# Kernel tuning notes

Hardware: AMD Instinct MI355X
Metric: run time of the kernel (lower is better)

The kernel has to match this reference:

```python
import jax, jax.numpy as jnp
import numpy as np

B, T, C = 1024, 256, 512
HEAD = 64

def setup_inputs() -> dict:
    key = jax.random.key(0)
    kx, kq, kk, kv = jax.random.split(key, 4)
    x = jax.random.normal(kx, (B, T, C), dtype=jnp.float32)
    # nn.Linear(n_embed, head_size, bias=False): y = x @ W where W is [C, head]
    s = 1.0 / np.sqrt(C)
    Wq = jax.random.normal(kq, (C, HEAD), dtype=jnp.float32) * s
    Wk = jax.random.normal(kk, (C, HEAD), dtype=jnp.float32) * s
    Wv = jax.random.normal(kv, (C, HEAD), dtype=jnp.float32) * s
    return {"x": x, "Wq": Wq, "Wk": Wk, "Wv": Wv}

def reference(x, Wq, Wk, Wv):
    # Naive single-head causal self-attention (dropout in eval mode = identity).
    T_ = x.shape[1]
    q = jnp.einsum('btc,ch->bth', x, Wq)
    k = jnp.einsum('btc,ch->bth', x, Wk)
    v = jnp.einsum('btc,ch->bth', x, Wv)
    scale = q.shape[-1] ** -0.5
    wei = jnp.einsum('bth,bsh->bts', q, k) * scale  # [B,T,T]
    causal = jnp.tril(jnp.ones((T_, T_), dtype=bool))
    wei = jnp.where(causal, wei, -jnp.inf)
    wei = jax.nn.softmax(wei, axis=-1)
    out = jnp.einsum('bts,bsh->bth', wei, v)  # [B,T,HEAD]
    return out
```

## Files before the change

### kernel.cpp

```cpp
#include <hip/hip_runtime.h>
#include <hip/hip_bf16.h>

#define NB 1024
#define NT 256
#define NC 512
#define NH 64

typedef __attribute__((ext_vector_type(8))) short bf16x8;
typedef __attribute__((ext_vector_type(4))) float f32x4;
typedef __attribute__((ext_vector_type(4))) short s16x4;
typedef __attribute__((ext_vector_type(4))) int   i32x4;

__device__ __forceinline__ short f2bf(float f) {
    unsigned u = __builtin_bit_cast(unsigned, f);
    u = (u + 0x7FFFu + ((u >> 16) & 1u)) >> 16;
    return (short)u;
}

__device__ __forceinline__ bf16x8 cvt8(f32x4 a0, f32x4 a1) {
#if defined(__has_builtin) && __has_builtin(__builtin_amdgcn_cvt_pk_bf16_f32)
    i32x4 pk;
    pk[0] = __builtin_bit_cast(int, __builtin_amdgcn_cvt_pk_bf16_f32(a0[0], a0[1]));
    pk[1] = __builtin_bit_cast(int, __builtin_amdgcn_cvt_pk_bf16_f32(a0[2], a0[3]));
    pk[2] = __builtin_bit_cast(int, __builtin_amdgcn_cvt_pk_bf16_f32(a1[0], a1[1]));
    pk[3] = __builtin_bit_cast(int, __builtin_amdgcn_cvt_pk_bf16_f32(a1[2], a1[3]));
    return __builtin_bit_cast(bf16x8, pk);
#else
    bf16x8 r;
    r[0] = f2bf(a0[0]); r[1] = f2bf(a0[1]); r[2] = f2bf(a0[2]); r[3] = f2bf(a0[3]);
    r[4] = f2bf(a1[0]); r[5] = f2bf(a1[1]); r[6] = f2bf(a1[2]); r[7] = f2bf(a1[3]);
    return r;
#endif
}

__global__ void swzw(const float* __restrict__ Wq, const float* __restrict__ Wk,
                     const float* __restrict__ Wv, short* __restrict__ wsw) {
    int tid = blockIdx.x * 256 + threadIdx.x;
    int j    = tid & 7;
    int l16  = (tid >> 3) & 15;
    int quad = (tid >> 7) & 3;
    int tgi  = (tid >> 9) & 3;
    int c    = (tid >> 11) & 15;
    int g2   = tid >> 15;
    const float* W = (g2 == 0) ? Wq : (g2 == 1) ? Wk : Wv;
    int h = tgi * 16 + l16;
    int k = c * 32 + quad * 8 + j;
    wsw[tid] = f2bf(W[k * NH + h]);
}

__global__ __launch_bounds__(512, 4)
void attn_fused(const float* __restrict__ x, const short* __restrict__ wsw,
                float* __restrict__ out) {
    __shared__ short lds[36864];
    const int b    = blockIdx.x;
    const int tid  = threadIdx.x;
    const int w    = tid >> 6;
    const int lane = tid & 63;
    const int l16  = lane & 15;
    const int quad = lane >> 4;

    const float* xb = x + (size_t)b * NT * NC;
    const int rts[2] = { w, 15 - w };

    short* pbw = lds + w * 512;
    const short* kb = lds + 4096;
    const short* vb = lds + 20480;

    bf16x8 qf[2][2];

    #pragma unroll
    for (int i = 0; i < 2; ++i) {
        const int R = rts[i];
        const float* xp = xb + (size_t)(R * 16 + l16) * NC + quad * 8;
        const short* wq = wsw + lane * 8;

        f32x4 acc[12];
        #pragma unroll
        for (int t = 0; t < 12; ++t) acc[t] = (f32x4){0.f, 0.f, 0.f, 0.f};

        f32x4 xa[2][2];
        xa[0][0] = *(const f32x4*)xp;
        xa[0][1] = *(const f32x4*)(xp + 4);

        #pragma unroll 2
        for (int c = 0; c < 16; ++c) {
            const int cur = c & 1;
            if (c < 15) {
                const float* pn = xp + (c + 1) * 32;
                xa[cur ^ 1][0] = *(const f32x4*)pn;
                xa[cur ^ 1][1] = *(const f32x4*)(pn + 4);
            }
            const short* wc = wq + c * 2048;
            bf16x8 af = cvt8(xa[cur][0], xa[cur][1]);
            {
                bf16x8 b0 = *(const bf16x8*)(wc);
                bf16x8 b1 = *(const bf16x8*)(wc + 512);
                bf16x8 b2 = *(const bf16x8*)(wc + 1024);
                bf16x8 b3 = *(const bf16x8*)(wc + 1536);
                acc[0] = __builtin_amdgcn_mfma_f32_16x16x32_bf16(af, b0, acc[0], 0, 0, 0);
                acc[1] = __builtin_amdgcn_mfma_f32_16x16x32_bf16(af, b1, acc[1], 0, 0, 0);
                acc[2] = __builtin_amdgcn_mfma_f32_16x16x32_bf16(af, b2, acc[2], 0, 0, 0);
                acc[3] = __builtin_amdgcn_mfma_f32_16x16x32_bf16(af, b3, acc[3], 0, 0, 0);
            }
            {
                bf16x8 b4 = *(const bf16x8*)(wc + 32768);
                bf16x8 b5 = *(const bf16x8*)(wc + 33280);
                bf16x8 b6 = *(const bf16x8*)(wc + 33792);
                bf16x8 b7 = *(const bf16x8*)(wc + 34304);
                acc[4] = __builtin_amdgcn_mfma_f32_16x16x32_bf16(af, b4, acc[4], 0, 0, 0);
                acc[5] = __builtin_amdgcn_mfma_f32_16x16x32_bf16(af, b5, acc[5], 0, 0, 0);
                acc[6] = __builtin_amdgcn_mfma_f32_16x16x32_bf16(af, b6, acc[6], 0, 0, 0);
                acc[7] = __builtin_amdgcn_mfma_f32_16x16x32_bf16(af, b7, acc[7], 0, 0, 0);
            }
            {
                bf16x8 b8  = *(const bf16x8*)(wc + 65536);
                bf16x8 b9  = *(const bf16x8*)(wc + 66048);
                bf16x8 b10 = *(const bf16x8*)(wc + 66560);
                bf16x8 b11 = *(const bf16x8*)(wc + 67072);
                acc[8]  = __builtin_amdgcn_mfma_f32_16x16x32_bf16(af, b8,  acc[8],  0, 0, 0);
                acc[9]  = __builtin_amdgcn_mfma_f32_16x16x32_bf16(af, b9,  acc[9],  0, 0, 0);
                acc[10] = __builtin_amdgcn_mfma_f32_16x16x32_bf16(af, b10, acc[10], 0, 0, 0);
                acc[11] = __builtin_amdgcn_mfma_f32_16x16x32_bf16(af, b11, acc[11], 0, 0, 0);
            }
        }

        #pragma unroll
        for (int hh = 0; hh < 2; ++hh) {
            #pragma unroll
            for (int t2 = 0; t2 < 2; ++t2) {
                const f32x4 a = acc[hh * 2 + t2];
                #pragma unroll
                for (int r = 0; r < 4; ++r)
                    pbw[(quad * 4 + r) * 32 + t2 * 16 + l16] = f2bf(a[r] * 0.125f);
            }
            qf[i][hh] = *(const bf16x8*)(pbw + l16 * 32 + quad * 8);
        }
        #pragma unroll
        for (int t2 = 0; t2 < 4; ++t2) {
            const int h = t2 * 16 + l16;
            const int koff = 4096 + R * 1024 + (h >> 5) * 512 + ((h >> 3) & 3) * 128 + (h & 7);
            const f32x4 a = acc[4 + t2];
            #pragma unroll
            for (int r = 0; r < 4; ++r)
                lds[koff + (quad * 4 + r) * 8] = f2bf(a[r]);
        }
        #pragma unroll
        for (int t2 = 0; t2 < 4; ++t2) {
            const int h = t2 * 16 + l16;
            const f32x4 a = acc[8 + t2];
            #pragma unroll
            for (int r = 0; r < 4; ++r) {
                const int row = R * 16 + quad * 4 + r;
                lds[20480 + (row >> 5) * 2048 + (h >> 4) * 512 + ((row >> 3) & 3) * 128
                    + (h & 15) * 8 + (row & 7)] = f2bf(a[r]);
            }
        }
    }
    __syncthreads();

    #pragma unroll
    for (int i = 0; i < 2; ++i) {
        const int R = rts[i];
        f32x4 sacc[16];
        #pragma unroll
        for (int ct = 0; ct < 16; ++ct) sacc[ct] = (f32x4){0.f, 0.f, 0.f, 0.f};

        #pragma unroll
        for (int ct = 0; ct < 16; ++ct) {
            if (ct <= R) {
                #pragma unroll
                for (int c = 0; c < 2; ++c) {
                    bf16x8 kf = *(const bf16x8*)(kb + ct * 1024 + c * 512 + quad * 128 + l16 * 8);
                    sacc[ct] = __builtin_amdgcn_mfma_f32_16x16x32_bf16(kf, qf[i][c], sacc[ct], 0, 0, 0);
                }
                if (ct == R) {
                    #pragma unroll
                    for (int r = 0; r < 4; ++r)
                        if (quad * 4 + r > l16) sacc[ct][r] = -1e30f;
                }
            }
        }

        f32x4 mm = (f32x4){-1e30f, -1e30f, -1e30f, -1e30f};
        #pragma unroll
        for (int ct = 0; ct < 16; ++ct)
            if (ct <= R) {
                #pragma unroll
                for (int r = 0; r < 4; ++r) mm[r] = fmaxf(mm[r], sacc[ct][r]);
            }
        float m0 = fmaxf(fmaxf(mm[0], mm[1]), fmaxf(mm[2], mm[3]));
        m0 = fmaxf(m0, __shfl_xor(m0, 16));
        m0 = fmaxf(m0, __shfl_xor(m0, 32));

        f32x4 lsv = (f32x4){0.f, 0.f, 0.f, 0.f};
        #pragma unroll
        for (int ct = 0; ct < 16; ++ct)
            if (ct <= R) {
                #pragma unroll
                for (int r = 0; r < 4; ++r) {
                    float p = __expf(sacc[ct][r] - m0);
                    sacc[ct][r] = p;
                    lsv[r] += p;
                }
            }
        float ls = (lsv[0] + lsv[1]) + (lsv[2] + lsv[3]);
        ls += __shfl_xor(ls, 16);
        ls += __shfl_xor(ls, 32);

        f32x4 oacc[4];
        #pragma unroll
        for (int ot = 0; ot < 4; ++ot) oacc[ot] = (f32x4){0.f, 0.f, 0.f, 0.f};

        #pragma unroll
        for (int c2 = 0; c2 < 8; ++c2) {
            if (c2 <= (R >> 1)) {
                #pragma unroll
                for (int half = 0; half < 2; ++half) {
                    int ct = 2 * c2 + half;
                    s16x4 vals;
                    if (ct <= R) {
                        #pragma unroll
                        for (int r = 0; r < 4; ++r) vals[r] = f2bf(sacc[ct][r]);
                    } else {
                        vals = (s16x4){0, 0, 0, 0};
                    }
                    *(s16x4*)(pbw + l16 * 32 + half * 16 + quad * 4) = vals;
                }
                bf16x8 pf = *(const bf16x8*)(pbw + l16 * 32 + quad * 8);
                #pragma unroll
                for (int ot = 0; ot < 4; ++ot) {
                    bf16x8 vf = *(const bf16x8*)(vb + c2 * 2048 + ot * 512 + quad * 128 + l16 * 8);
                    oacc[ot] = __builtin_amdgcn_mfma_f32_16x16x32_bf16(vf, pf, oacc[ot], 0, 0, 0);
                }
            }
        }

        float inv = 1.0f / ls;
        float* ob = out + ((size_t)b * NT + R * 16 + l16) * NH;
        #pragma unroll
        for (int ot = 0; ot < 4; ++ot) {
            f32x4 o;
            #pragma unroll
            for (int r = 0; r < 4; ++r) o[r] = oacc[ot][r] * inv;
            *(f32x4*)(ob + ot * 16 + quad * 4) = o;
        }
    }
}

extern "C" void kernel_launch(void* const* d_in, const int* in_sizes, int n_in,
                              void* d_out, int out_size, void* d_ws, size_t ws_size,
                              hipStream_t stream) {
    const float* x  = (const float*)d_in[0];
    const float* Wq = (const float*)d_in[1];
    const float* Wk = (const float*)d_in[2];
    const float* Wv = (const float*)d_in[3];
    float* outp = (float*)d_out;
    short* wsw  = (short*)d_ws;

    swzw<<<384, 256, 0, stream>>>(Wq, Wk, Wv, wsw);
    attn_fused<<<NB, 512, 0, stream>>>(x, wsw, outp);
}
```

Measured before the change: 776.5 us.

## Reuse weight fragments across both row tiles by splitting QKV projection into two passes

The projection phase is restructured so each wave processes both of its row tiles at once, loading each weight fragment once and feeding it to two MFMAs. The 12 output column tiles are split into two passes of six, and the weight buffer is re-swizzled into a pass-major layout so each pass reads contiguous fragments. This halves weight loads per wave and keeps the accumulator count at twelve, but x rows are now read twice (once per pass). The per-wave scratch stride is also padded from 32 to 40 shorts to cut LDS bank conflicts, which enlarges the shared buffer slightly.

```diff
diff --git a/kernel.cpp b/kernel.cpp
--- a/kernel.cpp
+++ b/kernel.cpp
@@ -39,10 +39,18 @@
     int j    = tid & 7;
     int l16  = (tid >> 3) & 15;
     int quad = (tid >> 7) & 3;
-    int tgi  = (tid >> 9) & 3;
-    int c    = (tid >> 11) & 15;
-    int g2   = tid >> 15;
-    const float* W = (g2 == 0) ? Wq : (g2 == 1) ? Wk : Wv;
+    int rest = tid >> 9;
+    int tl   = rest % 6;
+    int cp   = rest / 6;
+    int c    = cp & 15;
+    int pass = cp >> 4;
+    int g, tgi;
+    if (pass == 0) {
+        if (tl < 4) { g = 0; tgi = tl; } else { g = 1; tgi = tl - 4; }
+    } else {
+        if (tl < 2) { g = 1; tgi = tl + 2; } else { g = 2; tgi = tl - 2; }
+    }
+    const float* W = (g == 0) ? Wq : (g == 1) ? Wk : Wv;
     int h = tgi * 16 + l16;
     int k = c * 32 + quad * 8 + j;
     wsw[tid] = f2bf(W[k * NH + h]);
@@ -51,7 +59,7 @@
 __global__ __launch_bounds__(512, 4)
 void attn_fused(const float* __restrict__ x, const short* __restrict__ wsw,
                 float* __restrict__ out) {
-    __shared__ short lds[36864];
+    __shared__ short lds[37888];
     const int b    = blockIdx.x;
     const int tid  = threadIdx.x;
     const int w    = tid >> 6;
@@ -62,97 +70,124 @@
     const float* xb = x + (size_t)b * NT * NC;
     const int rts[2] = { w, 15 - w };
 
-    short* pbw = lds + w * 512;
-    const short* kb = lds + 4096;
-    const short* vb = lds + 20480;
+    short* pbw = lds + w * 640;
+    const short* kb = lds + 5120;
+    const short* vb = lds + 21504;
 
     bf16x8 qf[2][2];
 
+    const float* xp0 = xb + (size_t)(rts[0] * 16 + l16) * NC + quad * 8;
+    const float* xp1 = xb + (size_t)(rts[1] * 16 + l16) * NC + quad * 8;
+
     #pragma unroll
-    for (int i = 0; i < 2; ++i) {
-        const int R = rts[i];
-        const float* xp = xb + (size_t)(R * 16 + l16) * NC + quad * 8;
-        const short* wq = wsw + lane * 8;
-
-        f32x4 acc[12];
-        #pragma unroll
-        for (int t = 0; t < 12; ++t) acc[t] = (f32x4){0.f, 0.f, 0.f, 0.f};
-
-        f32x4 xa[2][2];
-        xa[0][0] = *(const f32x4*)xp;
-        xa[0][1] = *(const f32x4*)(xp + 4);
+    for (int pass = 0; pass < 2; ++pass) {
+        f32x4 acc[2][6];
+        #pragma unroll
+        for (int rt = 0; rt < 2; ++rt)
+            #pragma unroll
+            for (int t = 0; t < 6; ++t)
+                acc[rt][t] = (f32x4){0.f, 0.f, 0.f, 0.f};
+
+        const short* wp = wsw + pass * 49152 + lane * 8;
+
+        f32x4 xa[2][2][2];
+        xa[0][0][0] = *(const f32x4*)xp0;
+        xa[0][0][1] = *(const f32x4*)(xp0 + 4);
+        xa[0][1][0] = *(const f32x4*)xp1;
+        xa[0][1][1] = *(const f32x4*)(xp1 + 4);
 
         #pragma unroll 2
         for (int c = 0; c < 16; ++c) {
             const int cur = c & 1;
             if (c < 15) {
-                const float* pn = xp + (c + 1) * 32;
-                xa[cur ^ 1][0] = *(const f32x4*)pn;
-                xa[cur ^ 1][1] = *(const f32x4*)(pn + 4);
-            }
-            const short* wc = wq + c * 2048;
-            bf16x8 af = cvt8(xa[cur][0], xa[cur][1]);
+                const float* p0 = xp0 + (c + 1) * 32;
+                const float* p1 = xp1 + (c + 1) * 32;
+                xa[cur ^ 1][0][0] = *(const f32x4*)p0;
+                xa[cur ^ 1][0][1] = *(const f32x4*)(p0 + 4);
+                xa[cur ^ 1][1][0] = *(const f32x4*)p1;
+                xa[cur ^ 1][1][1] = *(const f32x4*)(p1 + 4);
+            }
+            const short* wc = wp + c * 3072;
+            bf16x8 af0 = cvt8(xa[cur][0][0], xa[cur][0][1]);
+            bf16x8 af1 = cvt8(xa[cur][1][0], xa[cur][1][1]);
             {
                 bf16x8 b0 = *(const bf16x8*)(wc);
                 bf16x8 b1 = *(const bf16x8*)(wc + 512);
+                acc[0][0] = __builtin_amdgcn_mfma_f32_16x16x32_bf16(af0, b0, acc[0][0], 0, 0, 0);
+                acc[1][0] = __builtin_amdgcn_mfma_f32_16x16x32_bf16(af1, b0, acc[1][0], 0, 0, 0);
+                acc[0][1] = __builtin_amdgcn_mfma_f32_16x16x32_bf16(af0, b1, acc[0][1], 0, 0, 0);
+                acc[1][1] = __builtin_amdgcn_mfma_f32_16x16x32_bf16(af1, b1, acc[1][1], 0, 0, 0);
+            }
+            {
                 bf16x8 b2 = *(const bf16x8*)(wc + 1024);
                 bf16x8 b3 = *(const bf16x8*)(wc + 1536);
-                acc[0] = __builtin_amdgcn_mfma_f32_16x16x32_bf16(af, b0, acc[0], 0, 0, 0);
-                acc[1] = __builtin_amdgcn_mfma_f32_16x16x32_bf16(af, b1, acc[1], 0, 0, 0);
-                acc[2] = __builtin_amdgcn_mfma_f32_16x16x32_bf16(af, b2, acc[2], 0, 0, 0);
-                acc[3] = __builtin_amdgcn_mfma_f32_16x16x32_bf16(af, b3, acc[3], 0, 0, 0);
+                acc[0][2] = __builtin_amdgcn_mfma_f32_16x16x32_bf16(af0, b2, acc[0][2], 0, 0, 0);
+                acc[1][2] = __builtin_amdgcn_mfma_f32_16x16x32_bf16(af1, b2, acc[1][2], 0, 0, 0);
+                acc[0][3] = __builtin_amdgcn_mfma_f32_16x16x32_bf16(af0, b3, acc[0][3], 0, 0, 0);
+                acc[1][3] = __builtin_amdgcn_mfma_f32_16x16x32_bf16(af1, b3, acc[1][3], 0, 0, 0);
             }
             {
-                bf16x8 b4 = *(const bf16x8*)(wc + 32768);
-                bf16x8 b5 = *(const bf16x8*)(wc + 33280);
-                bf16x8 b6 = *(const bf16x8*)(wc + 33792);
-                bf16x8 b7 = *(const bf16x8*)(wc + 34304);
-                acc[4] = __builtin_amdgcn_mfma_f32_16x16x32_bf16(af, b4, acc[4], 0, 0, 0);
-                acc[5] = __builtin_amdgcn_mfma_f32_16x16x32_bf16(af, b5, acc[5], 0, 0, 0);
-                acc[6] = __builtin_amdgcn_mfma_f32_16x16x32_bf16(af, b6, acc[6], 0, 0, 0);
-                acc[7] = __builtin_amdgcn_mfma_f32_16x16x32_bf16(af, b7, acc[7], 0, 0, 0);
-            }
-            {
-                bf16x8 b8  = *(const bf16x8*)(wc + 65536);
-                bf16x8 b9  = *(const bf16x8*)(wc + 66048);
-                bf16x8 b10 = *(const bf16x8*)(wc + 66560);
-                bf16x8 b11 = *(const bf16x8*)(wc + 67072);
-                acc[8]  = __builtin_amdgcn_mfma_f32_16x16x32_bf16(af, b8,  acc[8],  0, 0, 0);
-                acc[9]  = __builtin_amdgcn_mfma_f32_16x16x32_bf16(af, b9,  acc[9],  0, 0, 0);
-                acc[10] = __builtin_amdgcn_mfma_f32_16x16x32_bf16(af, b10, acc[10], 0, 0, 0);
-                acc[11] = __builtin_amdgcn_mfma_f32_16x16x32_bf16(af, b11, acc[11], 0, 0, 0);
-            }
-        }
-
-        #pragma unroll
-        for (int hh = 0; hh < 2; ++hh) {
-            #pragma unroll
-            for (int t2 = 0; t2 < 2; ++t2) {
-                const f32x4 a = acc[hh * 2 + t2];
-                #pragma unroll
-                for (int r = 0; r < 4; ++r)
-                    pbw[(quad * 4 + r) * 32 + t2 * 16 + l16] = f2bf(a[r] * 0.125f);
-            }
-            qf[i][hh] = *(const bf16x8*)(pbw + l16 * 32 + quad * 8);
-        }
-        #pragma unroll
-        for (int t2 = 0; t2 < 4; ++t2) {
-            const int h = t2 * 16 + l16;
-            const int koff = 4096 + R * 1024 + (h >> 5) * 512 + ((h >> 3) & 3) * 128 + (h & 7);
-            const f32x4 a = acc[4 + t2];
-            #pragma unroll
-            for (int r = 0; r < 4; ++r)
-                lds[koff + (quad * 4 + r) * 8] = f2bf(a[r]);
-        }
-        #pragma unroll
-        for (int t2 = 0; t2 < 4; ++t2) {
-            const int h = t2 * 16 + l16;
-            const f32x4 a = acc[8 + t2];
-            #pragma unroll
-            for (int r = 0; r < 4; ++r) {
-                const int row = R * 16 + quad * 4 + r;
-                lds[20480 + (row >> 5) * 2048 + (h >> 4) * 512 + ((row >> 3) & 3) * 128
-                    + (h & 15) * 8 + (row & 7)] = f2bf(a[r]);
+                bf16x8 b4 = *(const bf16x8*)(wc + 2048);
+                bf16x8 b5 = *(const bf16x8*)(wc + 2560);
+                acc[0][4] = __builtin_amdgcn_mfma_f32_16x16x32_bf16(af0, b4, acc[0][4], 0, 0, 0);
+                acc[1][4] = __builtin_amdgcn_mfma_f32_16x16x32_bf16(af1, b4, acc[1][4], 0, 0, 0);
+                acc[0][5] = __builtin_amdgcn_mfma_f32_16x16x32_bf16(af0, b5, acc[0][5], 0, 0, 0);
+                acc[1][5] = __builtin_amdgcn_mfma_f32_16x16x32_bf16(af1, b5, acc[1][5], 0, 0, 0);
+            }
+        }
+
+        if (pass == 0) {
+            #pragma unroll
+            for (int rt = 0; rt < 2; ++rt) {
+                #pragma unroll
+                for (int hh = 0; hh < 2; ++hh) {
+                    #pragma unroll
+                    for (int t2 = 0; t2 < 2; ++t2) {
+                        const f32x4 a = acc[rt][hh * 2 + t2];
+                        #pragma unroll
+                        for (int r = 0; r < 4; ++r)
+                            pbw[(quad * 4 + r) * 40 + t2 * 16 + l16] = f2bf(a[r] * 0.125f);
+                    }
+                    qf[rt][hh] = *(const bf16x8*)(pbw + l16 * 40 + quad * 8);
+                }
+            }
+            #pragma unroll
+            for (int rt = 0; rt < 2; ++rt) {
+                const int R = rts[rt];
+                #pragma unroll
+                for (int t2 = 0; t2 < 2; ++t2) {
+                    const int h = t2 * 16 + l16;
+                    const int koff = 5120 + R * 1024 + (h >> 5) * 512 + ((h >> 3) & 3) * 128 + (h & 7);
+                    const f32x4 a = acc[rt][4 + t2];
+                    #pragma unroll
+                    for (int r = 0; r < 4; ++r)
+                        lds[koff + (quad * 4 + r) * 8] = f2bf(a[r]);
+                }
+            }
+        } else {
+            #pragma unroll
+            for (int rt = 0; rt < 2; ++rt) {
+                const int R = rts[rt];
+                #pragma unroll
+                for (int t2 = 0; t2 < 2; ++t2) {
+                    const int h = 32 + t2 * 16 + l16;
+                    const int koff = 5120 + R * 1024 + (h >> 5) * 512 + ((h >> 3) & 3) * 128 + (h & 7);
+                    const f32x4 a = acc[rt][t2];
+                    #pragma unroll
+                    for (int r = 0; r < 4; ++r)
+                        lds[koff + (quad * 4 + r) * 8] = f2bf(a[r]);
+                }
+                #pragma unroll
+                for (int t2 = 0; t2 < 4; ++t2) {
+                    const int h = t2 * 16 + l16;
+                    const f32x4 a = acc[rt][2 + t2];
+                    #pragma unroll
+                    for (int r = 0; r < 4; ++r) {
+                        const int row = R * 16 + quad * 4 + r;
+                        lds[21504 + (row >> 5) * 2048 + (h >> 4) * 512 + ((row >> 3) & 3) * 128
+                            + (h & 15) * 8 + (row & 7)] = f2bf(a[r]);
+                    }
+                }
             }
         }
     }
@@ -224,9 +259,9 @@
                     } else {
                         vals = (s16x4){0, 0, 0, 0};
                     }
-                    *(s16x4*)(pbw + l16 * 32 + half * 16 + quad * 4) = vals;
-                }
-                bf16x8 pf = *(const bf16x8*)(pbw + l16 * 32 + quad * 8);
+                    *(s16x4*)(pbw + l16 * 40 + half * 16 + quad * 4) = vals;
+                }
+                bf16x8 pf = *(const bf16x8*)(pbw + l16 * 40 + quad * 8);
                 #pragma unroll
                 for (int ot = 0; ot < 4; ++ot) {
                     bf16x8 vf = *(const bf16x8*)(vb + c2 * 2048 + ot * 512 + quad * 128 + l16 * 8);
```

After: 809.1 us. +4.2%, slower.
